# Optimization experiments

Hardware: AMD Instinct MI355X
Metric: run time of the kernel (lower is better)

Reference implementation:

```python
import jax, jax.numpy as jnp
import numpy as np

B, L, D = 256, 512, 64          # batch, seq_length, input_size
HE, HD, S, NC = 1024, 1024, 24, 2  # hidden_enc, hidden_dec, steps, num_classes
ALPHA, BETA = 0.3, 0.5
COLS = jnp.array([1, 2])        # ES_Normalize columns


def _gru(x, h0, Wih, Whh, bih, bhh):
    """torch nn.GRU (1 layer, batch_first). x: [B,T,Din], h0: [B,H]."""
    def step(h, xt):
        gi = xt @ Wih.T + bih              # [B, 3H]
        gh = h @ Whh.T + bhh               # [B, 3H]
        ir, iz, inn = jnp.split(gi, 3, axis=-1)
        hr, hz, hn = jnp.split(gh, 3, axis=-1)
        r = jax.nn.sigmoid(ir + hr)
        z = jax.nn.sigmoid(iz + hz)
        n = jnp.tanh(inn + r * hn)
        h_new = (1.0 - z) * n + z * h
        return h_new, h_new
    hT, hs = jax.lax.scan(step, h0, jnp.swapaxes(x, 0, 1))
    return jnp.swapaxes(hs, 0, 1), hT      # [B,T,H], [B,H]


def _es_normalize(x, a):
    # torch version does x.clone().detach() -> gradient is cut here
    x = jax.lax.stop_gradient(x)
    def step(prev, xt):
        o = (1.0 - a) * xt + a * prev      # out[i] = (1-a)*x[i] + a*out[i-1]
        return o, o
    _, outs = jax.lax.scan(step, x[:, 0, :], jnp.swapaxes(x[:, 1:, :], 0, 1))
    out = jnp.concatenate([x[:, :1, :], jnp.swapaxes(outs, 0, 1)], axis=1)
    st = out[:, -1:, COLS]                 # pre_step=0 -> last step, columns [1,2]
    return out, st


def setup_inputs() -> dict:
    key = jax.random.key(0)
    ks = jax.random.split(key, 14)
    def u(k, shape, fan):
        b = 1.0 / np.sqrt(fan)
        return jax.random.uniform(k, shape, jnp.float32, -b, b)
    return {
        "x": jax.random.normal(ks[0], (B, L, D), jnp.float32),
        "enc_Wih": u(ks[1], (3 * HE, D), HE),
        "enc_Whh": u(ks[2], (3 * HE, HE), HE),
        "enc_bih": u(ks[3], (3 * HE,), HE),
        "enc_bhh": u(ks[4], (3 * HE,), HE),
        "dec_Wih": u(ks[5], (3 * HD, HE), HD),
        "dec_Whh": u(ks[6], (3 * HD, HD), HD),
        "dec_bih": u(ks[7], (3 * HD,), HD),
        "dec_bhh": u(ks[8], (3 * HD,), HD),
        "fci_W": u(ks[9], (HD, HE), HE),
        "fci_b": u(ks[10], (HD,), HE),
        "fc_W": u(ks[11], (NC, HD), HD),
        "fc_b": u(ks[12], (NC,), HD),
    }


def reference(x, enc_Wih, enc_Whh, enc_bih, enc_bhh,
              dec_Wih, dec_Whh, dec_bih, dec_bhh,
              fci_W, fci_b, fc_W, fc_b):
    b = x.shape[0]
    x1, st11 = _es_normalize(x, ALPHA)
    x2, st12 = _es_normalize(x1, BETA)
    h0 = jnp.zeros((b, HE), x.dtype)
    _, hT = _gru(x2, h0, enc_Wih, enc_Whh, enc_bih, enc_bhh)   # [B, HE]
    h0d = hT @ fci_W.T + fci_b                                  # fc_init_hidden_status
    # repeat + view: decoder input is encoder final state tiled over steps
    dec_in = jnp.broadcast_to(hT[:, None, :], (b, S, HE))
    dec_out, _ = _gru(dec_in, h0d, dec_Wih, dec_Whh, dec_bih, dec_bhh)  # [B,S,HD]
    out = dec_out @ fc_W.T + fc_b                               # [B, S, NC]
    # ES_DeNormalize: st is a snapshot (torch.cat copies), so the per-step loop
    # x[:,i]=(x[:,i]-a*st[:,i])/(1-a) is fully vectorizable.
    st2 = jnp.concatenate([st12, out[:, :S - 1, :]], axis=1)
    out = (out - BETA * st2) / (1.0 - BETA)
    st1 = jnp.concatenate([st11, out[:, :S - 1, :]], axis=1)
    out = (out - ALPHA * st1) / (1.0 - ALPHA)
    return out.reshape(b, S * NC)
```

## Files before the change

kernel.cpp:

```cpp
#include <hip/hip_runtime.h>

typedef _Float16 half8  __attribute__((ext_vector_type(8)));
typedef _Float16 half4v __attribute__((ext_vector_type(4)));
typedef float    float4v __attribute__((ext_vector_type(4)));

#define MFMA16(a, b, c) __builtin_amdgcn_mfma_f32_16x16x32_f16((a), (b), (c), 0, 0, 0)

constexpr int BB = 256;
constexpr int LL = 512;
constexpr int DD = 64;
constexpr int HH = 1024;
constexpr int SS = 24;

constexpr size_t OFF_X2    = 0;
constexpr size_t SZ_X2     = (size_t)BB * LL * DD * 2;
constexpr size_t OFF_HBUF  = OFF_X2 + SZ_X2;
constexpr size_t SZ_HBUF   = (size_t)2 * BB * HH * 2;
constexpr size_t OFF_OUTP  = OFF_HBUF + SZ_HBUF;
constexpr size_t SZ_OUTP   = (size_t)BB * SS * 2 * 4;
constexpr size_t OFF_BAR   = OFF_OUTP + SZ_OUTP;
constexpr size_t SZ_BAR    = 32 * 4;
constexpr size_t OFF_EFLAG = OFF_BAR + SZ_BAR;
constexpr size_t SZ_EFLAG  = (size_t)8 * 32 * 16 * 4;
constexpr size_t OFF_ST11  = OFF_EFLAG + SZ_EFLAG;
constexpr size_t OFF_ST12  = OFF_ST11 + 2048;
constexpr size_t OFF_FLAG  = OFF_ST12 + 2048;

__device__ __forceinline__ void agstore_u64(void* p, unsigned long long v) {
  __hip_atomic_store((unsigned long long*)p, v, __ATOMIC_RELAXED, __HIP_MEMORY_SCOPE_AGENT);
}
__device__ __forceinline__ void agstore_u32(void* p, unsigned v) {
  __hip_atomic_store((unsigned*)p, v, __ATOMIC_RELAXED, __HIP_MEMORY_SCOPE_AGENT);
}
__device__ __forceinline__ unsigned agload_u32(const unsigned* p) {
  return __hip_atomic_load(p, __ATOMIC_RELAXED, __HIP_MEMORY_SCOPE_AGENT);
}
__device__ __forceinline__ half8 agload_h8(const _Float16* p) {
  const unsigned long long* q = (const unsigned long long*)p;
  union { unsigned long long u[2]; half8 h; } cv;
  cv.u[0] = __hip_atomic_load(q,     __ATOMIC_RELAXED, __HIP_MEMORY_SCOPE_AGENT);
  cv.u[1] = __hip_atomic_load(q + 1, __ATOMIC_RELAXED, __HIP_MEMORY_SCOPE_AGENT);
  return cv.h;
}
__device__ __forceinline__ void agstore_h4(void* p, half4v h) {
  union { half4v h; unsigned long long u; } cv; cv.h = h;
  agstore_u64(p, cv.u);
}

template <int M, int N>
__device__ __forceinline__ void zero_acc(float4v (&a)[M][N]) {
  #pragma unroll
  for (int m = 0; m < M; ++m) {
    #pragma unroll
    for (int n = 0; n < N; ++n) {
      #pragma unroll
      for (int r = 0; r < 4; ++r) a[m][n][r] = 0.f;
    }
  }
}

__device__ __forceinline__ half8 ld_w8_f16(const float* p) {
  float4 f0 = *(const float4*)(p);
  float4 f1 = *(const float4*)(p + 4);
  half8 h;
  h[0] = (_Float16)f0.x; h[1] = (_Float16)f0.y; h[2] = (_Float16)f0.z; h[3] = (_Float16)f0.w;
  h[4] = (_Float16)f1.x; h[5] = (_Float16)f1.y; h[6] = (_Float16)f1.z; h[7] = (_Float16)f1.w;
  return h;
}

__device__ __forceinline__ void load_W_frags(const float* __restrict__ W, int s, int w,
                                             int lane, half8 BW[6][8]) {
  const int l15 = lane & 15, lq = lane >> 4;
  #pragma unroll
  for (int n = 0; n < 6; ++n) {
    const int row = (n >> 1) * 1024 + s * 32 + (n & 1) * 16 + l15;
    const float* rp = W + (size_t)row * HH + (w << 8) + (lq << 3);
    #pragma unroll
    for (int ks = 0; ks < 8; ++ks) BW[n][ks] = ld_w8_f16(rp + ks * 32);
  }
}

__device__ __forceinline__ void bar_arrive(unsigned* ef, int lb, unsigned ep1) {
  __syncthreads();
  if (threadIdx.x == 0) agstore_u32(&ef[lb * 16], ep1);
}
__device__ __forceinline__ void bar_wait(unsigned* ef, unsigned ep) {
  if (threadIdx.x < 32) {
    while (agload_u32(&ef[threadIdx.x * 16]) < ep)
      __builtin_amdgcn_s_sleep(1);
  }
  __syncthreads();
}

__device__ __forceinline__ void flag_barrier(unsigned* flags, int blk, int tid, unsigned val) {
  __syncthreads();
  if (tid == 0) agstore_u32(&flags[blk], val);
  while (agload_u32(&flags[tid]) != val)
    __builtin_amdgcn_s_sleep(2);
  __syncthreads();
}

#define PS(rw, cl) (P[(rw)*97 + (cl)] + P[3104 + (rw)*97 + (cl)] + \
                    P[6208 + (rw)*97 + (cl)] + P[9312 + (rw)*97 + (cl)])

__global__ __launch_bounds__(256, 1) void ts_fused(
    const float* __restrict__ x,
    const float* __restrict__ eWih, const float* __restrict__ eWhh,
    const float* __restrict__ ebih, const float* __restrict__ ebhh,
    const float* __restrict__ dWih, const float* __restrict__ dWhh,
    const float* __restrict__ dbih, const float* __restrict__ dbhh,
    const float* __restrict__ fciW, const float* __restrict__ fcib,
    const float* __restrict__ fcW,  const float* __restrict__ fcb,
    float* __restrict__ out, char* __restrict__ ws) {
  __shared__ float P[4 * 32 * 97];
  __shared__ float Q[32 * 97];

  _Float16* x2     = (_Float16*)(ws + OFF_X2);
  _Float16* hbuf   = (_Float16*)(ws + OFF_HBUF);
  float* outp      = (float*)(ws + OFF_OUTP);
  unsigned* bar    = (unsigned*)(ws + OFF_BAR);
  unsigned* eflags = (unsigned*)(ws + OFF_EFLAG);
  float* st11      = (float*)(ws + OFF_ST11);
  float* st12      = (float*)(ws + OFF_ST12);
  unsigned* flags  = (unsigned*)(ws + OFF_FLAG);

  const int tid  = threadIdx.x;
  const int blk  = blockIdx.x;
  const int lane = tid & 63;
  const int w    = tid >> 6;
  const int l15  = lane & 15;
  const int lq   = lane >> 4;
  const int g    = blk & 7;
  const int s    = blk >> 3;
  const int eb   = tid >> 3;
  const int jq   = tid & 7;
  const int colb = s * 32 + jq * 4;

  if (blk < 64) {
    if (tid < 64) {
      const int idx = blk * 64 + tid;
      const int b = idx >> 4, dq = idx & 15, d = dq * 4;
      const float* xp = x + (size_t)b * LL * DD + d;
      _Float16* x2p = x2 + (size_t)b * LL * DD + d;
      float v1[4] = {0.f, 0.f, 0.f, 0.f}, v2[4] = {0.f, 0.f, 0.f, 0.f};
      #pragma unroll 1
      for (int t = 0; t < LL; ++t) {
        const float4 xv = *(const float4*)(xp + (size_t)t * DD);
        const float xe[4] = {xv.x, xv.y, xv.z, xv.w};
        half4v hv;
        #pragma unroll
        for (int e = 0; e < 4; ++e) {
          v1[e] = (t == 0) ? xe[e] : 0.7f * xe[e] + 0.3f * v1[e];
          v2[e] = (t == 0) ? v1[e] : 0.5f * v1[e] + 0.5f * v2[e];
          hv[e] = (_Float16)v2[e];
        }
        agstore_h4(x2p + (size_t)t * DD, hv);
      }
      if (dq == 0) {
        union { float f[2]; unsigned long long u; } c1, c2;
        c1.f[0] = v1[1]; c1.f[1] = v1[2];
        c2.f[0] = v2[1]; c2.f[1] = v2[2];
        agstore_u64(&st11[b * 2], c1.u);
        agstore_u64(&st12[b * 2], c2.u);
      }
    }
  } else {
    unsigned long long* zr = (unsigned long long*)(ws + OFF_HBUF);
    const int NZ = (int)((SZ_HBUF + SZ_OUTP + SZ_BAR + SZ_EFLAG) / 8);
    for (int i = (blk - 64) * 256 + tid; i < NZ; i += 192 * 256) agstore_u64(&zr[i], 0ull);
  }

  flag_barrier(flags, blk, tid, 1u);

  unsigned* ef      = eflags + g * 32 * 16;
  unsigned* gridbar = bar;

  half8 BW[6][8];
  load_W_frags(eWhh, s, w, lane, BW);
  half8 BWi[6][2];
  if (w == 0) {
    #pragma unroll
    for (int n = 0; n < 6; ++n) {
      const int row = (n >> 1) * 1024 + s * 32 + (n & 1) * 16 + l15;
      const float* rp = eWih + (size_t)row * DD + (lq << 3);
      #pragma unroll
      for (int ks = 0; ks < 2; ++ks) BWi[n][ks] = ld_w8_f16(rp + ks * 32);
    }
  }
  float ebr[4], ebz[4], ebin[4], ebhn[4];
  #pragma unroll
  for (int e = 0; e < 4; ++e) {
    const int c = colb + e;
    ebr[e]  = ebih[c] + ebhh[c];
    ebz[e]  = ebih[1024 + c] + ebhh[1024 + c];
    ebin[e] = ebih[2048 + c];
    ebhn[e] = ebhh[2048 + c];
  }
  float hold[4] = {0.f, 0.f, 0.f, 0.f};

  #pragma unroll 1
  for (int t = 0; t < LL; ++t) {
    const _Float16* hc = hbuf + (size_t)(t & 1) * BB * HH;
    _Float16* hnx = hbuf + (size_t)((t + 1) & 1) * BB * HH;

    float4v acc[2][6], accI[2][2];
    zero_acc(acc);
    zero_acc(accI);

    if (w == 0) {
      #pragma unroll
      for (int ks = 0; ks < 2; ++ks) {
        const _Float16* ap = x2 + (size_t)(g * 32 + l15) * (LL * DD) + (size_t)t * DD + ks * 32 + (lq << 3);
        half8 a0 = *(const half8*)ap;
        half8 a1 = *(const half8*)(ap + (size_t)16 * LL * DD);
        #pragma unroll
        for (int n = 0; n < 6; ++n) {
          if (n < 4) {
            acc[0][n] = MFMA16(a0, BWi[n][ks], acc[0][n]);
            acc[1][n] = MFMA16(a1, BWi[n][ks], acc[1][n]);
          } else {
            accI[0][n - 4] = MFMA16(a0, BWi[n][ks], accI[0][n - 4]);
            accI[1][n - 4] = MFMA16(a1, BWi[n][ks], accI[1][n - 4]);
          }
        }
      }
    }
    if (t > 0) bar_wait(ef, (unsigned)t);
    #pragma unroll
    for (int ks = 0; ks < 8; ++ks) {
      const _Float16* ap = hc + (size_t)(g * 32 + l15) * HH + (w << 8) + ks * 32 + (lq << 3);
      half8 a0 = agload_h8(ap);
      half8 a1 = agload_h8(ap + 16 * HH);
      #pragma unroll
      for (int n = 0; n < 6; ++n) {
        acc[0][n] = MFMA16(a0, BW[n][ks], acc[0][n]);
        acc[1][n] = MFMA16(a1, BW[n][ks], acc[1][n]);
      }
    }
    {
      float* Pw = P + w * 3104;
      #pragma unroll
      for (int m = 0; m < 2; ++m) {
        const int row0 = m * 16 + lq * 4;
        #pragma unroll
        for (int n = 0; n < 6; ++n) {
          const int col = (n >> 1) * 32 + (n & 1) * 16 + l15;
          #pragma unroll
          for (int r = 0; r < 4; ++r) Pw[(row0 + r) * 97 + col] = acc[m][n][r];
        }
      }
      if (w == 0) {
        #pragma unroll
        for (int m = 0; m < 2; ++m) {
          const int row0 = m * 16 + lq * 4;
          #pragma unroll
          for (int n2 = 0; n2 < 2; ++n2) {
            const int col = n2 * 16 + l15;
            #pragma unroll
            for (int r = 0; r < 4; ++r) Q[(row0 + r) * 97 + col] = accI[m][n2][r];
          }
        }
      }
    }
    __syncthreads();
    {
      half4v hh;
      #pragma unroll
      for (int e = 0; e < 4; ++e) {
        const int j = jq * 4 + e;
        const float Sr = PS(eb, j);
        const float Sz = PS(eb, 32 + j);
        const float Hn = PS(eb, 64 + j);
        const float rr = 1.f / (1.f + __expf(-(Sr + ebr[e])));
        const float zz = 1.f / (1.f + __expf(-(Sz + ebz[e])));
        const float aN = (Q[eb * 97 + j] + ebin[e]) + rr * (Hn + ebhn[e]);
        const float nn = 1.f - 2.f / (1.f + __expf(2.f * aN));
        const float hv = (1.f - zz) * nn + zz * hold[e];
        hold[e] = hv;
        hh[e] = (_Float16)hv;
      }
      agstore_h4(hnx + (size_t)(g * 32 + eb) * HH + s * 32 + jq * 4, hh);
    }
    bar_arrive(ef, s, (unsigned)(t + 1));
  }

  {
    bar_wait(ef, (unsigned)LL);
    const _Float16* hT = hbuf;
    float4v acc[2][6];
    zero_acc(acc);
    #pragma unroll 1
    for (int ks = 0; ks < 8; ++ks) {
      const _Float16* ap = hT + (size_t)(g * 32 + l15) * HH + (w << 8) + ks * 32 + (lq << 3);
      half8 a0 = agload_h8(ap);
      half8 a1 = agload_h8(ap + 16 * HH);
      #pragma unroll
      for (int n = 0; n < 6; ++n) {
        const int row = (n >> 1) * 1024 + s * 32 + (n & 1) * 16 + l15;
        half8 bf = ld_w8_f16(dWih + (size_t)row * HH + (w << 8) + ks * 32 + (lq << 3));
        acc[0][n] = MFMA16(a0, bf, acc[0][n]);
        acc[1][n] = MFMA16(a1, bf, acc[1][n]);
      }
    }
    {
      float* Pw = P + w * 3104;
      #pragma unroll
      for (int m = 0; m < 2; ++m) {
        const int row0 = m * 16 + lq * 4;
        #pragma unroll
        for (int n = 0; n < 6; ++n) {
          const int col = (n >> 1) * 32 + (n & 1) * 16 + l15;
          #pragma unroll
          for (int r = 0; r < 4; ++r) Pw[(row0 + r) * 97 + col] = acc[m][n][r];
        }
      }
    }
    __syncthreads();
    #pragma unroll
    for (int e = 0; e < 4; ++e) {
      const int j = jq * 4 + e;
      #pragma unroll
      for (int gate = 0; gate < 3; ++gate) {
        const int col = gate * 32 + j;
        Q[eb * 97 + col] = PS(eb, col) + dbih[gate * 1024 + s * 32 + j];
      }
    }
    __syncthreads();
    float4v acc2[2][2];
    zero_acc(acc2);
    #pragma unroll 1
    for (int ks = 0; ks < 8; ++ks) {
      const _Float16* ap = hT + (size_t)(g * 32 + l15) * HH + (w << 8) + ks * 32 + (lq << 3);
      half8 a0 = agload_h8(ap);
      half8 a1 = agload_h8(ap + 16 * HH);
      #pragma unroll
      for (int n2 = 0; n2 < 2; ++n2) {
        const int row = s * 32 + n2 * 16 + l15;
        half8 bf = ld_w8_f16(fciW + (size_t)row * HH + (w << 8) + ks * 32 + (lq << 3));
        acc2[0][n2] = MFMA16(a0, bf, acc2[0][n2]);
        acc2[1][n2] = MFMA16(a1, bf, acc2[1][n2]);
      }
    }
    {
      float* Pw = P + w * 3104;
      #pragma unroll
      for (int m = 0; m < 2; ++m) {
        const int row0 = m * 16 + lq * 4;
        #pragma unroll
        for (int n2 = 0; n2 < 2; ++n2) {
          const int col = n2 * 16 + l15;
          #pragma unroll
          for (int r = 0; r < 4; ++r) Pw[(row0 + r) * 97 + col] = acc2[m][n2][r];
        }
      }
    }
    __syncthreads();
    {
      half4v hh;
      #pragma unroll
      for (int e = 0; e < 4; ++e) {
        const int j = jq * 4 + e;
        const float v = PS(eb, j) + fcib[s * 32 + j];
        hold[e] = v;
        hh[e] = (_Float16)v;
      }
      agstore_h4(hbuf + (size_t)BB * HH + (size_t)(g * 32 + eb) * HH + s * 32 + jq * 4, hh);
    }
    bar_arrive(ef, s, (unsigned)(LL + 1));
  }

  load_W_frags(dWhh, s, w, lane, BW);
  float dbr_[4], dbz_[4], dbn_[4], fw0[4], fw1[4];
  #pragma unroll
  for (int e = 0; e < 4; ++e) {
    const int c = colb + e;
    dbr_[e] = dbhh[c];
    dbz_[e] = dbhh[1024 + c];
    dbn_[e] = dbhh[2048 + c];
    fw0[e] = fcW[c];
    fw1[e] = fcW[1024 + c];
  }
  #pragma unroll 1
  for (int t = 0; t < SS; ++t) {
    bar_wait(ef, (unsigned)(LL + 1 + t));
    const _Float16* hc = hbuf + (size_t)((t + 1) & 1) * BB * HH;
    _Float16* hnx = hbuf + (size_t)(t & 1) * BB * HH;
    float4v acc[2][6];
    zero_acc(acc);
    #pragma unroll
    for (int ks = 0; ks < 8; ++ks) {
      const _Float16* ap = hc + (size_t)(g * 32 + l15) * HH + (w << 8) + ks * 32 + (lq << 3);
      half8 a0 = agload_h8(ap);
      half8 a1 = agload_h8(ap + 16 * HH);
      #pragma unroll
      for (int n = 0; n < 6; ++n) {
        acc[0][n] = MFMA16(a0, BW[n][ks], acc[0][n]);
        acc[1][n] = MFMA16(a1, BW[n][ks], acc[1][n]);
      }
    }
    {
      float* Pw = P + w * 3104;
      #pragma unroll
      for (int m = 0; m < 2; ++m) {
        const int row0 = m * 16 + lq * 4;
        #pragma unroll
        for (int n = 0; n < 6; ++n) {
          const int col = (n >> 1) * 32 + (n & 1) * 16 + l15;
          #pragma unroll
          for (int r = 0; r < 4; ++r) Pw[(row0 + r) * 97 + col] = acc[m][n][r];
        }
      }
    }
    __syncthreads();
    {
      half4v hh;
      float p0 = 0.f, p1 = 0.f;
      #pragma unroll
      for (int e = 0; e < 4; ++e) {
        const int j = jq * 4 + e;
        const float rr = 1.f / (1.f + __expf(-(PS(eb, j) + Q[eb * 97 + j] + dbr_[e])));
        const float zz = 1.f / (1.f + __expf(-(PS(eb, 32 + j) + Q[eb * 97 + 32 + j] + dbz_[e])));
        const float aN = Q[eb * 97 + 64 + j] + rr * (PS(eb, 64 + j) + dbn_[e]);
        const float nn = 1.f - 2.f / (1.f + __expf(2.f * aN));
        const float hv = (1.f - zz) * nn + zz * hold[e];
        hold[e] = hv;
        hh[e] = (_Float16)hv;
        p0 += hv * fw0[e];
        p1 += hv * fw1[e];
      }
      agstore_h4(hnx + (size_t)(g * 32 + eb) * HH + s * 32 + jq * 4, hh);
      p0 += __shfl_xor(p0, 1); p0 += __shfl_xor(p0, 2); p0 += __shfl_xor(p0, 4);
      p1 += __shfl_xor(p1, 1); p1 += __shfl_xor(p1, 2); p1 += __shfl_xor(p1, 4);
      if (jq == 0) {
        atomicAdd(&outp[((g * 32 + eb) * SS + t) * 2 + 0], p0);
        atomicAdd(&outp[((g * 32 + eb) * SS + t) * 2 + 1], p1);
      }
    }
    bar_arrive(ef, s, (unsigned)(LL + 2 + t));
  }

  bar_wait(ef, (unsigned)(LL + 1 + SS));
  if (s == 0 && tid == 0) atomicAdd(gridbar, 1u);
  if (tid == 0) {
    while (agload_u32(gridbar) < 8u) __builtin_amdgcn_s_sleep(1);
  }
  __syncthreads();

  if (blk < 2) {
    const int t5 = blk * 256 + tid;
    const int b = t5 >> 1, c = t5 & 1;
    const float s2v = st12[b * 2 + c];
    const float s1v = st11[b * 2 + c];
    const float bias = fcb[c];
    float o0p = 0.f, o1p = 0.f;
    #pragma unroll 1
    for (int t = 0; t < SS; ++t) {
      const float o0 = outp[(b * SS + t) * 2 + c] + bias;
      const float o1 = 2.f * o0 - ((t == 0) ? s2v : o0p);
      const float o2 = (o1 - 0.3f * ((t == 0) ? s1v : o1p)) * (1.f / 0.7f);
      o0p = o0; o1p = o1;
      out[b * 48 + t * 2 + c] = o2;
    }
  }

  if (tid == 0) agstore_u32(&flags[blk], 0u);
}

extern "C" void kernel_launch(void* const* d_in, const int* in_sizes, int n_in,
                              void* d_out, int out_size, void* d_ws, size_t ws_size,
                              hipStream_t stream) {
  (void)in_sizes; (void)n_in; (void)out_size; (void)ws_size;
  const float* x    = (const float*)d_in[0];
  const float* eWih = (const float*)d_in[1];
  const float* eWhh = (const float*)d_in[2];
  const float* ebih = (const float*)d_in[3];
  const float* ebhh = (const float*)d_in[4];
  const float* dWih = (const float*)d_in[5];
  const float* dWhh = (const float*)d_in[6];
  const float* dbih = (const float*)d_in[7];
  const float* dbhh = (const float*)d_in[8];
  const float* fciW = (const float*)d_in[9];
  const float* fcib = (const float*)d_in[10];
  const float* fcW  = (const float*)d_in[11];
  const float* fcb  = (const float*)d_in[12];
  float* out = (float*)d_out;
  char* ws = (char*)d_ws;

  ts_fused<<<dim3(256), dim3(256), 0, stream>>>(
      x, eWih, eWhh, ebih, ebhh, dWih, dWhh, dbih, dbhh,
      fciW, fcib, fcW, fcb, out, ws);
}
```

Measured before the change: 3.667 ms.

## Replace block-wide flag wait with per-wave wait on only needed producer blocks

Each wave now polls only the 8 producer blocks whose hidden-state slice it consumes, rather than the whole block waiting on all 32 flags and then hitting __syncthreads. The eight h-chunk loads are issued up front into registers before the MFMA loop, and the same registers are reused for both the decoder input-projection and the fci matmuls. This narrows the dependency in the recurrent step and removes one block barrier per step, at the cost of more live registers. Correctness depends on the wave-to-producer mapping matching the column slices each wave reads.

```diff
diff --git a/kernel.cpp b/kernel.cpp
--- a/kernel.cpp
+++ b/kernel.cpp
@@ -80,10 +80,23 @@
   }
 }
 
-__device__ __forceinline__ void bar_arrive(unsigned* ef, int lb, unsigned ep1) {
-  __syncthreads();
-  if (threadIdx.x == 0) agstore_u32(&ef[lb * 16], ep1);
-}
+__device__ __forceinline__ void wave_wait8(const unsigned* ef, int w, int lane, unsigned ep) {
+  if (lane < 8) {
+    const unsigned* fp = &ef[(w * 8 + lane) * 16];
+    while (agload_u32(fp) < ep) __builtin_amdgcn_s_sleep(1);
+  }
+}
+
+__device__ __forceinline__ void load_h_chunks(const _Float16* hc, int g, int w,
+                                              int l15, int lq, half8 A0[8], half8 A1[8]) {
+  const _Float16* base = hc + (size_t)(g * 32 + l15) * HH + (w << 8) + (lq << 3);
+  #pragma unroll
+  for (int ks = 0; ks < 8; ++ks) {
+    A0[ks] = agload_h8(base + ks * 32);
+    A1[ks] = agload_h8(base + ks * 32 + 16 * HH);
+  }
+}
+
 __device__ __forceinline__ void bar_wait(unsigned* ef, unsigned ep) {
   if (threadIdx.x < 32) {
     while (agload_u32(&ef[threadIdx.x * 16]) < ep)
@@ -225,16 +238,15 @@
         }
       }
     }
-    if (t > 0) bar_wait(ef, (unsigned)t);
+    wave_wait8(ef, w, lane, (unsigned)t);
+    half8 A0[8], A1[8];
+    load_h_chunks(hc, g, w, l15, lq, A0, A1);
     #pragma unroll
     for (int ks = 0; ks < 8; ++ks) {
-      const _Float16* ap = hc + (size_t)(g * 32 + l15) * HH + (w << 8) + ks * 32 + (lq << 3);
-      half8 a0 = agload_h8(ap);
-      half8 a1 = agload_h8(ap + 16 * HH);
       #pragma unroll
       for (int n = 0; n < 6; ++n) {
-        acc[0][n] = MFMA16(a0, BW[n][ks], acc[0][n]);
-        acc[1][n] = MFMA16(a1, BW[n][ks], acc[1][n]);
+        acc[0][n] = MFMA16(A0[ks], BW[n][ks], acc[0][n]);
+        acc[1][n] = MFMA16(A1[ks], BW[n][ks], acc[1][n]);
       }
     }
     {
@@ -281,25 +293,25 @@
       }
       agstore_h4(hnx + (size_t)(g * 32 + eb) * HH + s * 32 + jq * 4, hh);
     }
-    bar_arrive(ef, s, (unsigned)(t + 1));
+    __syncthreads();
+    if (tid == 0) agstore_u32(&ef[s * 16], (unsigned)(t + 1));
   }
 
   {
-    bar_wait(ef, (unsigned)LL);
     const _Float16* hT = hbuf;
+    wave_wait8(ef, w, lane, (unsigned)LL);
+    half8 A0[8], A1[8];
+    load_h_chunks(hT, g, w, l15, lq, A0, A1);
     float4v acc[2][6];
     zero_acc(acc);
     #pragma unroll 1
     for (int ks = 0; ks < 8; ++ks) {
-      const _Float16* ap = hT + (size_t)(g * 32 + l15) * HH + (w << 8) + ks * 32 + (lq << 3);
-      half8 a0 = agload_h8(ap);
-      half8 a1 = agload_h8(ap + 16 * HH);
       #pragma unroll
       for (int n = 0; n < 6; ++n) {
         const int row = (n >> 1) * 1024 + s * 32 + (n & 1) * 16 + l15;
         half8 bf = ld_w8_f16(dWih + (size_t)row * HH + (w << 8) + ks * 32 + (lq << 3));
-        acc[0][n] = MFMA16(a0, bf, acc[0][n]);
-        acc[1][n] = MFMA16(a1, bf, acc[1][n]);
+        acc[0][n] = MFMA16(A0[ks], bf, acc[0][n]);
+        acc[1][n] = MFMA16(A1[ks], bf, acc[1][n]);
       }
     }
     {
@@ -330,15 +342,12 @@
     zero_acc(acc2);
     #pragma unroll 1
     for (int ks = 0; ks < 8; ++ks) {
-      const _Float16* ap = hT + (size_t)(g * 32 + l15) * HH + (w << 8) + ks * 32 + (lq << 3);
-      half8 a0 = agload_h8(ap);
-      half8 a1 = agload_h8(ap + 16 * HH);
       #pragma unroll
       for (int n2 = 0; n2 < 2; ++n2) {
         const int row = s * 32 + n2 * 16 + l15;
         half8 bf = ld_w8_f16(fciW + (size_t)row * HH + (w << 8) + ks * 32 + (lq << 3));
-        acc2[0][n2] = MFMA16(a0, bf, acc2[0][n2]);
-        acc2[1][n2] = MFMA16(a1, bf, acc2[1][n2]);
+        acc2[0][n2] = MFMA16(A0[ks], bf, acc2[0][n2]);
+        acc2[1][n2] = MFMA16(A1[ks], bf, acc2[1][n2]);
       }
     }
     {
@@ -366,7 +375,8 @@
       }
       agstore_h4(hbuf + (size_t)BB * HH + (size_t)(g * 32 + eb) * HH + s * 32 + jq * 4, hh);
     }
-    bar_arrive(ef, s, (unsigned)(LL + 1));
+    __syncthreads();
+    if (tid == 0) agstore_u32(&ef[s * 16], (unsigned)(LL + 1));
   }
 
   load_W_frags(dWhh, s, w, lane, BW);
@@ -382,20 +392,19 @@
   }
   #pragma unroll 1
   for (int t = 0; t < SS; ++t) {
-    bar_wait(ef, (unsigned)(LL + 1 + t));
     const _Float16* hc = hbuf + (size_t)((t + 1) & 1) * BB * HH;
     _Float16* hnx = hbuf + (size_t)(t & 1) * BB * HH;
     float4v acc[2][6];
     zero_acc(acc);
+    wave_wait8(ef, w, lane, (unsigned)(LL + 1 + t));
+    half8 A0[8], A1[8];
+    load_h_chunks(hc, g, w, l15, lq, A0, A1);
     #pragma unroll
     for (int ks = 0; ks < 8; ++ks) {
-      const _Float16* ap = hc + (size_t)(g * 32 + l15) * HH + (w << 8) + ks * 32 + (lq << 3);
-      half8 a0 = agload_h8(ap);
-      half8 a1 = agload_h8(ap + 16 * HH);
       #pragma unroll
       for (int n = 0; n < 6; ++n) {
-        acc[0][n] = MFMA16(a0, BW[n][ks], acc[0][n]);
-        acc[1][n] = MFMA16(a1, BW[n][ks], acc[1][n]);
+        acc[0][n] = MFMA16(A0[ks], BW[n][ks], acc[0][n]);
+        acc[1][n] = MFMA16(A1[ks], BW[n][ks], acc[1][n]);
       }
     }
     {
@@ -436,7 +445,8 @@
         atomicAdd(&outp[((g * 32 + eb) * SS + t) * 2 + 1], p1);
       }
     }
-    bar_arrive(ef, s, (unsigned)(LL + 2 + t));
+    __syncthreads();
+    if (tid == 0) agstore_u32(&ef[s * 16], (unsigned)(LL + 2 + t));
   }
 
   bar_wait(ef, (unsigned)(LL + 1 + SS));
```

Measured after the change: 3.708 ms. About the same (+1.1%).
